# Performance work log

Hardware: AMD Instinct MI355X
Metric: run time of the kernel (lower is better)

## Reference

```python
import jax, jax.numpy as jnp
import numpy as np

B, S, H = 2, 1024, 2048
NH, NOPE, ROPE, VD = 16, 128, 64, 128
QKD = NOPE + ROPE  # 192
QLR, KVLR = 1536, 512
EPS = 1e-5


def _ln(x, w):
    # torch F.layer_norm with weight, no bias
    m = jnp.mean(x, axis=-1, keepdims=True)
    v = jnp.mean(jnp.square(x - m), axis=-1, keepdims=True)
    return (x - m) * jax.lax.rsqrt(v + EPS) * w


def _rope(x, cos, sin):
    x1, x2 = jnp.split(x, 2, axis=-1)
    return x * cos + jnp.concatenate((-x2, x1), axis=-1) * sin


def setup_inputs() -> dict:
    key = jax.random.key(0)
    ks = jax.random.split(key, 10)
    sd = 0.02
    return {
        "hidden_states": jax.random.normal(ks[0], (B, S, H), jnp.float32),
        "cos": jax.random.uniform(ks[1], (B, S, ROPE), jnp.float32),
        "sin": jax.random.uniform(ks[2], (B, S, ROPE), jnp.float32),
        "w_qa": jax.random.normal(ks[3], (QLR, H), jnp.float32) * sd,
        "q_a_ln_w": jnp.ones((QLR,), jnp.float32),
        "w_qb": jax.random.normal(ks[4], (NH * QKD, QLR), jnp.float32) * sd,
        "w_kva": jax.random.normal(ks[5], (KVLR + ROPE, H), jnp.float32) * sd,
        "kv_a_ln_w": jnp.ones((KVLR,), jnp.float32),
        "W_UK_T": jax.random.normal(ks[6], (NH, NOPE, KVLR), jnp.float32) * sd,
        "W_UV": jax.random.normal(ks[7], (NH, KVLR, VD), jnp.float32) * sd,
        "w_o": jax.random.normal(ks[8], (H, NH * VD), jnp.float32) * sd,
    }


def reference(hidden_states, cos, sin, w_qa, q_a_ln_w, w_qb, w_kva, kv_a_ln_w,
              W_UK_T, W_UV, w_o):
    b, s, _ = hidden_states.shape
    # fused mlapo: low-rank Q path + LN + RoPE
    qa = _ln(hidden_states @ w_qa.T, q_a_ln_w)            # [b,s,QLR]
    q = (qa @ w_qb.T).reshape(b, s, NH, QKD)              # [b,s,h,192]
    q_nope, q_pe = q[..., :NOPE], q[..., NOPE:]
    q_pe = _rope(q_pe, cos[:, :, None, :], sin[:, :, None, :])
    # KV low-rank path (MQA latent) + LN + RoPE on shared k_pe
    kva = hidden_states @ w_kva.T                          # [b,s,KVLR+ROPE]
    kv_c = _ln(kva[..., :KVLR], kv_a_ln_w)                 # [b,s,KVLR]
    k_pe = _rope(kva[..., KVLR:], cos, sin)                # [b,s,ROPE]
    # absorbed latent attention
    q_lat = jnp.einsum('bshd,hdl->bshl', q_nope, W_UK_T)   # [b,s,h,KVLR]
    scores = (jnp.einsum('bqhl,bkl->bhqk', q_lat, kv_c)
              + jnp.einsum('bqhr,bkr->bhqk', q_pe, k_pe)) * (1.0 / np.sqrt(QKD))
    mask = jnp.tril(jnp.ones((s, s), bool))
    scores = jnp.where(mask, scores, jnp.finfo(scores.dtype).min)
    p = jax.nn.softmax(scores, axis=-1)                    # [b,h,q,k]
    ctx = jnp.einsum('bhqk,bkl->bqhl', p, kv_c)            # [b,s,h,KVLR]
    out = jnp.einsum('bqhl,hlv->bqhv', ctx, W_UV)          # [b,s,h,VD]
    return out.reshape(b, s, NH * VD) @ w_o.T              # [b,s,H]
```

## Files before the change

### kernel.cpp

```cpp
#include <hip/hip_runtime.h>
#include <hip/hip_bf16.h>
#include <math.h>

#define BB 2
#define SS 1024
#define HH 2048
#define NHD 16
#define NOPE 128
#define ROPED 64
#define VDIM 128
#define QKD 192
#define QLR 1536
#define KVLR 512
#define EPSF 1e-5f
#define NCOMB 2176

typedef __bf16 bf16x8 __attribute__((ext_vector_type(8)));
typedef float  f32x4  __attribute__((ext_vector_type(4)));

__device__ __forceinline__ void gload_lds16(const __bf16* g, __bf16* l) {
    __builtin_amdgcn_global_load_lds(
        (const __attribute__((address_space(1))) void*)g,
        (__attribute__((address_space(3))) void*)l, 16, 0, 0);
}

__device__ __forceinline__ void swz2d(int nx, int ny, int& bx, int& by) {
    int T = nx * ny;
    int lin = blockIdx.x + nx * blockIdx.y;
    if ((T & 7) == 0) {
        int q = T >> 3;
        lin = (lin & 7) * q + (lin >> 3);
    }
    bx = lin % nx;
    by = lin / nx;
}

template<int BK>
__device__ __forceinline__ void gemm_core_dbuf(
    const __bf16* __restrict__ Ab, const __bf16* __restrict__ Bb,
    int lda, int ldb, int m0, int n0, int K, __bf16* lds, f32x4 acc[4][4])
{
    constexpr int CH    = BK / 8;
    constexpr int LPT   = CH / 2;
    constexpr int BUFE  = 256 * BK;
    constexpr int BOFF  = 128 * BK;
    constexpr int RSTEP = 2048 / BK;
    const int tid = threadIdx.x;
    const int w = tid >> 6, lane = tid & 63, quad = lane >> 4, ln = lane & 15;
    const int wm = (w >> 1) * 64, wn = (w & 1) * 64;
    const int nt = K / BK;

    const int sr  = tid / CH;
    const int spc = tid % CH;
    const int sc  = (BK == 64) ? (spc ^ (sr & 7)) : (spc ^ ((sr >> 1) & 3));
    const __bf16* gA = Ab + (size_t)(m0 + sr) * lda + sc * 8;
    const __bf16* gB = Bb + (size_t)(n0 + sr) * ldb + sc * 8;

    const int swm = (BK == 64) ? ((wm + ln) & 7) : (((wm + ln) >> 1) & 3);
    const int swn = (BK == 64) ? ((wn + ln) & 7) : (((wn + ln) >> 1) & 3);

    auto stage = [&](int buf, int kk) {
        __bf16* la = lds + buf * BUFE + w * 512;
        __bf16* lb = la + BOFF;
        const __bf16* ga = gA + kk;
        const __bf16* gb = gB + kk;
#pragma unroll
        for (int i = 0; i < LPT; ++i) {
            gload_lds16(ga + (size_t)(i * RSTEP) * lda, la + i * 2048);
            gload_lds16(gb + (size_t)(i * RSTEP) * ldb, lb + i * 2048);
        }
    };
    auto wait_stage = [&]() {
        if constexpr (BK == 64) asm volatile("s_waitcnt vmcnt(8)" ::: "memory");
        else                    asm volatile("s_waitcnt vmcnt(4)" ::: "memory");
    };

    stage(0, 0);
    stage(1, BK);
    wait_stage();
    __builtin_amdgcn_s_barrier();
    __builtin_amdgcn_sched_barrier(0);

    for (int t = 0; t < nt; ++t) {
        const int cur = t & 1;
        const __bf16* bufA = lds + cur * BUFE;
        const __bf16* bufB = bufA + BOFF;
        bf16x8 af[BK / 32][4], bv[BK / 32][4];
#pragma unroll
        for (int ks = 0; ks < BK / 32; ++ks)
#pragma unroll
            for (int i = 0; i < 4; ++i) {
                af[ks][i] = *(const bf16x8*)
                    &bufA[(wm + ln) * BK + i * 16 * BK + (((ks * 4 + quad) ^ swm) << 3)];
                bv[ks][i] = *(const bf16x8*)
                    &bufB[(wn + ln) * BK + i * 16 * BK + (((ks * 4 + quad) ^ swn) << 3)];
            }
        __builtin_amdgcn_s_setprio(1);
#pragma unroll
        for (int ks = 0; ks < BK / 32; ++ks)
#pragma unroll
            for (int mi = 0; mi < 4; ++mi)
#pragma unroll
                for (int ni = 0; ni < 4; ++ni)
                    acc[mi][ni] = __builtin_amdgcn_mfma_f32_16x16x32_bf16(
                        af[ks][mi], bv[ks][ni], acc[mi][ni], 0, 0, 0);
        __builtin_amdgcn_s_setprio(0);
        if (t + 1 < nt) {
            __builtin_amdgcn_sched_barrier(0);
            asm volatile("" ::: "memory");
            __builtin_amdgcn_s_barrier();
            asm volatile("" ::: "memory");
            if (t + 2 < nt) {
                stage(cur, (t + 2) * BK);
                wait_stage();
            } else {
                asm volatile("s_waitcnt vmcnt(0)" ::: "memory");
            }
            __builtin_amdgcn_s_barrier();
            __builtin_amdgcn_sched_barrier(0);
        }
    }
}

template<int BK>
__device__ __forceinline__ void gemm_core_tri(
    const __bf16* __restrict__ Ab, const __bf16* __restrict__ Bb,
    int lda, int ldb, int m0, int n0, int K, __bf16* lds, f32x4 acc[4][4])
{
    constexpr int CH    = BK / 8;
    constexpr int LPT   = CH / 2;
    constexpr int BUFE  = 256 * BK;
    constexpr int BOFF  = 128 * BK;
    constexpr int RSTEP = 2048 / BK;
    const int tid = threadIdx.x;
    const int w = tid >> 6, lane = tid & 63, quad = lane >> 4, ln = lane & 15;
    const int wm = (w >> 1) * 64, wn = (w & 1) * 64;
    const int nt = K / BK;

    const int sr  = tid / CH;
    const int spc = tid % CH;
    const int sc  = (BK == 64) ? (spc ^ (sr & 7)) : (spc ^ ((sr >> 1) & 3));
    const __bf16* gA = Ab + (size_t)(m0 + sr) * lda + sc * 8;
    const __bf16* gB = Bb + (size_t)(n0 + sr) * ldb + sc * 8;

    const int swm = (BK == 64) ? ((wm + ln) & 7) : (((wm + ln) >> 1) & 3);
    const int swn = (BK == 64) ? ((wn + ln) & 7) : (((wn + ln) >> 1) & 3);

    auto stage = [&](__bf16* base, int kk) {
        __bf16* la = base + w * 512;
        __bf16* lb = la + BOFF;
        const __bf16* ga = gA + kk;
        const __bf16* gb = gB + kk;
#pragma unroll
        for (int i = 0; i < LPT; ++i) {
            gload_lds16(ga + (size_t)(i * RSTEP) * lda, la + i * 2048);
            gload_lds16(gb + (size_t)(i * RSTEP) * ldb, lb + i * 2048);
        }
    };

    __bf16* p0 = lds;
    __bf16* p1 = lds + BUFE;
    __bf16* p2 = lds + 2 * BUFE;

    stage(p0, 0);
    stage(p1, BK);
    if constexpr (BK == 64) asm volatile("s_waitcnt vmcnt(8)" ::: "memory");
    else                    asm volatile("s_waitcnt vmcnt(4)" ::: "memory");
    __builtin_amdgcn_s_barrier();
    __builtin_amdgcn_sched_barrier(0);

    for (int t = 0; t < nt; ++t) {
        if (t + 2 < nt) stage(p2, (t + 2) * BK);
        bf16x8 af[BK / 32][4], bv[BK / 32][4];
#pragma unroll
        for (int ks = 0; ks < BK / 32; ++ks)
#pragma unroll
            for (int i = 0; i < 4; ++i) {
                af[ks][i] = *(const bf16x8*)
                    &p0[(wm + ln) * BK + i * 16 * BK + (((ks * 4 + quad) ^ swm) << 3)];
                bv[ks][i] = *(const bf16x8*)
                    &p0[BOFF + (wn + ln) * BK + i * 16 * BK + (((ks * 4 + quad) ^ swn) << 3)];
            }
        __builtin_amdgcn_s_setprio(1);
#pragma unroll
        for (int ks = 0; ks < BK / 32; ++ks)
#pragma unroll
            for (int mi = 0; mi < 4; ++mi)
#pragma unroll
                for (int ni = 0; ni < 4; ++ni)
                    acc[mi][ni] = __builtin_amdgcn_mfma_f32_16x16x32_bf16(
                        af[ks][mi], bv[ks][ni], acc[mi][ni], 0, 0, 0);
        __builtin_amdgcn_s_setprio(0);
        if (t + 1 < nt) {
            __builtin_amdgcn_sched_barrier(0);
            if (t + 2 < nt) {
                if constexpr (BK == 64) asm volatile("s_waitcnt vmcnt(8)" ::: "memory");
                else                    asm volatile("s_waitcnt vmcnt(4)" ::: "memory");
            } else {
                asm volatile("s_waitcnt vmcnt(0)" ::: "memory");
            }
            __builtin_amdgcn_s_barrier();
            __builtin_amdgcn_sched_barrier(0);
        }
        __bf16* tmp = p0; p0 = p1; p1 = p2; p2 = tmp;
    }
}

template<bool OUT_BF16, int BK, int MINW, bool TRI>
__global__ __launch_bounds__(256, MINW) void gemm_mfma(
    const __bf16* __restrict__ A, const __bf16* __restrict__ B, void* __restrict__ Cv,
    int M, int N, int K, int lda, int ldb, int ldc,
    long long sA, long long sB, long long sC)
{
    __shared__ __bf16 lds[TRI ? 768 * BK : 512 * BK];
    const __bf16* Ab = A + (long long)blockIdx.z * sA;
    const __bf16* Bb = B + (long long)blockIdx.z * sB;
    const int tid = threadIdx.x;
    const int w = tid >> 6, lane = tid & 63, quad = lane >> 4, ln = lane & 15;
    int bx, by; swz2d(gridDim.x, gridDim.y, bx, by);
    const int m0 = by * 128, n0 = bx * 128;
    const int wm = (w >> 1) * 64, wn = (w & 1) * 64;

    f32x4 acc[4][4];
#pragma unroll
    for (int i = 0; i < 4; ++i)
#pragma unroll
        for (int j = 0; j < 4; ++j) acc[i][j] = (f32x4){0.f, 0.f, 0.f, 0.f};

    if (TRI) gemm_core_tri<BK>(Ab, Bb, lda, ldb, m0, n0, K, lds, acc);
    else     gemm_core_dbuf<BK>(Ab, Bb, lda, ldb, m0, n0, K, lds, acc);

    if (OUT_BF16) {
        __bf16* Cb = (__bf16*)Cv + (long long)blockIdx.z * sC;
#pragma unroll
        for (int mi = 0; mi < 4; ++mi)
#pragma unroll
            for (int r = 0; r < 4; ++r) {
                size_t row = (size_t)(m0 + wm + mi * 16 + quad * 4 + r);
#pragma unroll
                for (int ni = 0; ni < 4; ++ni)
                    Cb[row * ldc + (n0 + wn + ni * 16 + ln)] = (__bf16)acc[mi][ni][r];
            }
    } else {
        float* Cb = (float*)Cv + (long long)blockIdx.z * sC;
#pragma unroll
        for (int mi = 0; mi < 4; ++mi)
#pragma unroll
            for (int r = 0; r < 4; ++r) {
                size_t row = (size_t)(m0 + wm + mi * 16 + quad * 4 + r);
#pragma unroll
                for (int ni = 0; ni < 4; ++ni)
                    Cb[row * ldc + (n0 + wn + ni * 16 + ln)] = acc[mi][ni][r];
            }
    }
}

__global__ __launch_bounds__(256, 3) void gemm_qlat(
    const __bf16* __restrict__ qb, const __bf16* __restrict__ Wkb,
    __bf16* __restrict__ Qc)
{
    __shared__ __bf16 lds[768 * 32];
    const int h = blockIdx.z;
    const __bf16* Ab = qb + (size_t)h * QKD;
    const __bf16* Bb = Wkb + (size_t)h * KVLR * NOPE;
    const int tid = threadIdx.x;
    const int w = tid >> 6, lane = tid & 63, quad = lane >> 4, ln = lane & 15;
    int bx, by; swz2d(gridDim.x, gridDim.y, bx, by);
    const int m0 = by * 128, n0 = bx * 128;
    const int wm = (w >> 1) * 64, wn = (w & 1) * 64;

    f32x4 acc[4][4];
#pragma unroll
    for (int i = 0; i < 4; ++i)
#pragma unroll
        for (int j = 0; j < 4; ++j) acc[i][j] = (f32x4){0.f, 0.f, 0.f, 0.f};

    gemm_core_tri<32>(Ab, Bb, NHD * QKD, NOPE, m0, n0, NOPE, lds, acc);

#pragma unroll
    for (int mi = 0; mi < 4; ++mi)
#pragma unroll
        for (int r = 0; r < 4; ++r) {
            int row = m0 + wm + mi * 16 + quad * 4 + r;
            int bb = row >> 10, s = row & 1023;
            __bf16* dst = Qc + ((size_t)(bb * NHD + h) * SS + s) * 576;
#pragma unroll
            for (int ni = 0; ni < 4; ++ni)
                dst[n0 + wn + ni * 16 + ln] = (__bf16)acc[mi][ni][r];
        }
}

__global__ __launch_bounds__(256, 3) void gemm_vh(
    const __bf16* __restrict__ Wvb, const __bf16* __restrict__ Kc,
    __bf16* __restrict__ Vh)
{
    int lin = blockIdx.x + 8 * blockIdx.z;
    lin = (lin & 7) * 32 + (lin >> 3);
    const int z = lin >> 3;
    const int ntile = lin & 7;
    const int b = z >> 4, h = z & 15;

    __shared__ __bf16 lds[768 * 32];
    const __bf16* Ab = Wvb + (size_t)h * VDIM * KVLR;
    const __bf16* Bb = Kc + (size_t)b * SS * 576;
    const int tid = threadIdx.x;
    const int w = tid >> 6, lane = tid & 63, quad = lane >> 4, ln = lane & 15;
    const int m0 = 0, n0 = ntile * 128;
    const int wm = (w >> 1) * 64, wn = (w & 1) * 64;

    f32x4 acc[4][4];
#pragma unroll
    for (int i = 0; i < 4; ++i)
#pragma unroll
        for (int j = 0; j < 4; ++j) acc[i][j] = (f32x4){0.f, 0.f, 0.f, 0.f};

    gemm_core_tri<32>(Ab, Bb, KVLR, 576, m0, n0, KVLR, lds, acc);

    __bf16* Cb = Vh + (size_t)z * VDIM * SS;
#pragma unroll
    for (int mi = 0; mi < 4; ++mi)
#pragma unroll
        for (int r = 0; r < 4; ++r) {
            int row = m0 + wm + mi * 16 + quad * 4 + r;
#pragma unroll
            for (int ni = 0; ni < 4; ++ni)
                Cb[(size_t)row * SS + (n0 + wn + ni * 16 + ln)] = (__bf16)acc[mi][ni][r];
        }
}

__global__ __launch_bounds__(256, 3) void gemm_scores(
    const __bf16* __restrict__ Qc, const __bf16* __restrict__ Kc,
    __bf16* __restrict__ Sc)
{
    int lin = blockIdx.x + 36 * blockIdx.y;
    lin = (lin & 7) * 144 + (lin >> 3);
    const int z = lin / 36;
    const int i = lin - z * 36;
    int mt = (int)((sqrtf(8.f * i + 1.f) - 1.f) * 0.5f);
    if (mt * (mt + 1) / 2 > i) --mt;
    if ((mt + 1) * (mt + 2) / 2 <= i) ++mt;
    const int nt = i - mt * (mt + 1) / 2;

    const int b = z >> 4;
    __shared__ __bf16 lds[768 * 32];
    const __bf16* Ab = Qc + (size_t)z * SS * 576;
    const __bf16* Bb = Kc + (size_t)b * SS * 576;
    __bf16* Cb = Sc + (size_t)z * SS * SS;
    const int tid = threadIdx.x;
    const int w = tid >> 6, lane = tid & 63, quad = lane >> 4, ln = lane & 15;
    const int m0 = mt * 128, n0 = nt * 128;
    const int wm = (w >> 1) * 64, wn = (w & 1) * 64;

    f32x4 acc[4][4];
#pragma unroll
    for (int i2 = 0; i2 < 4; ++i2)
#pragma unroll
        for (int j = 0; j < 4; ++j) acc[i2][j] = (f32x4){0.f, 0.f, 0.f, 0.f};

    gemm_core_tri<32>(Ab, Bb, 576, 576, m0, n0, 576, lds, acc);

    const float SCL2 = 0.07216878364870323f * 1.4426950408889634f;
#pragma unroll
    for (int mi = 0; mi < 4; ++mi)
#pragma unroll
        for (int r = 0; r < 4; ++r) {
            int row = m0 + wm + mi * 16 + quad * 4 + r;
#pragma unroll
            for (int ni = 0; ni < 4; ++ni) {
                int col = n0 + wn + ni * 16 + ln;
                float v = acc[mi][ni][r] * SCL2;
                if (col > row) v = -1e30f;
                Cb[(size_t)row * SS + col] = (__bf16)v;
            }
        }
}

__global__ __launch_bounds__(256) void softmax_kernel(__bf16* __restrict__ Sc)
{
    const int z = blockIdx.y;
    const int w = threadIdx.x >> 6, lane = threadIdx.x & 63;
    const int r = blockIdx.x * 4 + w;
    __bf16* row = Sc + (size_t)z * SS * SS + (size_t)r * SS;
    const int ncols = ((r >> 7) + 1) << 7;
    const int i0 = lane * 8, i1 = i0 + 512;
    const bool a0 = i0 < ncols, a1 = i1 < ncols;
    float v[16];
    float lmax = -1e30f;
    if (a0) {
        bf16x8 c = *(const bf16x8*)(row + i0);
#pragma unroll
        for (int j = 0; j < 8; ++j) { v[j] = (float)c[j]; lmax = fmaxf(lmax, v[j]); }
    }
    if (a1) {
        bf16x8 c = *(const bf16x8*)(row + i1);
#pragma unroll
        for (int j = 0; j < 8; ++j) { v[8 + j] = (float)c[j]; lmax = fmaxf(lmax, v[8 + j]); }
    }
#pragma unroll
    for (int off = 1; off < 64; off <<= 1) lmax = fmaxf(lmax, __shfl_xor(lmax, off));
    float lsum = 0.f;
    if (a0) {
#pragma unroll
        for (int j = 0; j < 8; ++j) { v[j] = __builtin_amdgcn_exp2f(v[j] - lmax); lsum += v[j]; }
    }
    if (a1) {
#pragma unroll
        for (int j = 0; j < 8; ++j) { v[8 + j] = __builtin_amdgcn_exp2f(v[8 + j] - lmax); lsum += v[8 + j]; }
    }
#pragma unroll
    for (int off = 1; off < 64; off <<= 1) lsum += __shfl_xor(lsum, off);
    const float inv = 1.f / lsum;
    if (a0) {
        bf16x8 c;
#pragma unroll
        for (int j = 0; j < 8; ++j) c[j] = (__bf16)(v[j] * inv);
        *(bf16x8*)(row + i0) = c;
    }
    if (a1) {
        bf16x8 c;
#pragma unroll
        for (int j = 0; j < 8; ++j) c[j] = (__bf16)(v[8 + j] * inv);
        *(bf16x8*)(row + i1) = c;
    }
}

__global__ __launch_bounds__(256, 3) void gemm_pv(
    const __bf16* __restrict__ Sc, const __bf16* __restrict__ Vh,
    __bf16* __restrict__ ohb)
{
    int lin = blockIdx.x + 8 * blockIdx.y;
    lin = (lin & 7) * 32 + (lin >> 3);
    const int z = lin >> 3;
    const int mt = lin & 7;

    const int b = z >> 4, h = z & 15;
    const int Keff = (mt + 1) * 128;
    __shared__ __bf16 lds[768 * 32];
    const __bf16* Ab = Sc + (size_t)z * SS * SS;
    const __bf16* Bb = Vh + (size_t)z * VDIM * SS;
    const int tid = threadIdx.x;
    const int w = tid >> 6, lane = tid & 63, quad = lane >> 4, ln = lane & 15;
    const int m0 = mt * 128, n0 = 0;
    const int wm = (w >> 1) * 64, wn = (w & 1) * 64;

    f32x4 acc[4][4];
#pragma unroll
    for (int i = 0; i < 4; ++i)
#pragma unroll
        for (int j = 0; j < 4; ++j) acc[i][j] = (f32x4){0.f, 0.f, 0.f, 0.f};

    gemm_core_tri<32>(Ab, Bb, SS, SS, m0, n0, Keff, lds, acc);

#pragma unroll
    for (int mi = 0; mi < 4; ++mi)
#pragma unroll
        for (int r = 0; r < 4; ++r) {
            int row = m0 + wm + mi * 16 + quad * 4 + r;
            __bf16* op = ohb + (size_t)(b * SS + row) * (NHD * VDIM) + h * VDIM;
#pragma unroll
            for (int ni = 0; ni < 4; ++ni)
                op[n0 + wn + ni * 16 + ln] = (__bf16)acc[mi][ni][r];
        }
}

__global__ __launch_bounds__(256) void castf2b(const float* __restrict__ in,
                                               __bf16* __restrict__ out, int n)
{
    int i = (blockIdx.x * 256 + threadIdx.x) * 4;
    if (i < n) {
        float4 v = *(const float4*)(in + i);
        out[i] = (__bf16)v.x; out[i + 1] = (__bf16)v.y;
        out[i + 2] = (__bf16)v.z; out[i + 3] = (__bf16)v.w;
    }
}

__global__ __launch_bounds__(256) void cast_comb(const float* __restrict__ wqa,
                                                 const float* __restrict__ wkva,
                                                 __bf16* __restrict__ out)
{
    int idx = (blockIdx.x * 256 + threadIdx.x) * 4;
    int row = idx >> 11, col = idx & 2047;
    const float* src;
    if (row < 1536)      src = wqa + (size_t)row * 2048 + col;
    else if (row < 2112) src = wkva + (size_t)(row - 1536) * 2048 + col;
    else {
        out[idx] = (__bf16)0.f; out[idx + 1] = (__bf16)0.f;
        out[idx + 2] = (__bf16)0.f; out[idx + 3] = (__bf16)0.f;
        return;
    }
    float4 v = *(const float4*)src;
    out[idx] = (__bf16)v.x; out[idx + 1] = (__bf16)v.y;
    out[idx + 2] = (__bf16)v.z; out[idx + 3] = (__bf16)v.w;
}

__global__ __launch_bounds__(256) void transpose_cast(const float* __restrict__ in,
                                                      __bf16* __restrict__ out,
                                                      int R, int C)
{
    __shared__ float t[32][33];
    in  += (size_t)blockIdx.z * R * C;
    out += (size_t)blockIdx.z * R * C;
    int c0 = blockIdx.x * 32, r0 = blockIdx.y * 32;
    int tx = threadIdx.x & 31, ty = threadIdx.x >> 5;
#pragma unroll
    for (int i = 0; i < 4; ++i) {
        int r = ty + i * 8;
        t[r][tx] = in[(size_t)(r0 + r) * C + c0 + tx];
    }
    __syncthreads();
#pragma unroll
    for (int i = 0; i < 4; ++i) {
        int rr = ty + i * 8;
        out[(size_t)(c0 + rr) * R + r0 + tx] = (__bf16)t[tx][rr];
    }
}

__global__ __launch_bounds__(256) void ln_kernel(const float* __restrict__ x,
                                                 const float* __restrict__ w,
                                                 __bf16* __restrict__ y, int N, int ldx)
{
    long long row = blockIdx.x;
    const float* xr = x + row * ldx;
    __bf16* yr = y + row * N;
    int tid = threadIdx.x;
    float s = 0.f, ss = 0.f;
    for (int i = tid; i < N; i += 256) { float v = xr[i]; s += v; ss += v * v; }
#pragma unroll
    for (int off = 32; off > 0; off >>= 1) { s += __shfl_down(s, off); ss += __shfl_down(ss, off); }
    __shared__ float rs[4], rss[4];
    __shared__ float smean, sinv;
    int wave = tid >> 6, lane = tid & 63;
    if (lane == 0) { rs[wave] = s; rss[wave] = ss; }
    __syncthreads();
    if (tid == 0) {
        float S = rs[0] + rs[1] + rs[2] + rs[3];
        float Q = rss[0] + rss[1] + rss[2] + rss[3];
        float mean = S / N;
        float var = Q / N - mean * mean;
        smean = mean; sinv = rsqrtf(var + EPSF);
    }
    __syncthreads();
    float mean = smean, inv = sinv;
    for (int i = tid; i < N; i += 256) yr[i] = (__bf16)((xr[i] - mean) * inv * w[i]);
}

__global__ __launch_bounds__(256) void prep_kernel(
    const float* __restrict__ kva, int ld, const float* __restrict__ kvw,
    const float* __restrict__ cosb, const float* __restrict__ sinb,
    __bf16* __restrict__ Kc, const __bf16* __restrict__ q,
    __bf16* __restrict__ Qc)
{
    long long row = blockIdx.x;
    const float* kr = kva + row * ld;
    const float* cr = cosb + row * ROPED;
    const float* sr = sinb + row * ROPED;
    int tid = threadIdx.x;
    float v0 = kr[tid], v1 = kr[tid + 256];
    float s = v0 + v1, ss = v0 * v0 + v1 * v1;
#pragma unroll
    for (int off = 32; off > 0; off >>= 1) { s += __shfl_down(s, off); ss += __shfl_down(ss, off); }
    __shared__ float rs[4], rss[4];
    __shared__ float smean, sinv;
    int wave = tid >> 6, lane = tid & 63;
    if (lane == 0) { rs[wave] = s; rss[wave] = ss; }
    __syncthreads();
    if (tid == 0) {
        float S = rs[0] + rs[1] + rs[2] + rs[3];
        float Q = rss[0] + rss[1] + rss[2] + rss[3];
        float mean = S / KVLR;
        float var = Q / KVLR - mean * mean;
        smean = mean; sinv = rsqrtf(var + EPSF);
    }
    __syncthreads();
    float mean = smean, inv = sinv;
    __bf16* kc = Kc + row * 576;
    kc[tid]       = (__bf16)((v0 - mean) * inv * kvw[tid]);
    kc[tid + 256] = (__bf16)((v1 - mean) * inv * kvw[tid + 256]);
    if (tid < 32) {
        float x1 = kr[KVLR + tid], x2 = kr[KVLR + 32 + tid];
        kc[512 + tid]      = (__bf16)(x1 * cr[tid] - x2 * sr[tid]);
        kc[512 + 32 + tid] = (__bf16)(x2 * cr[32 + tid] + x1 * sr[32 + tid]);
    }
    const int bb = (int)(row >> 10), sp = (int)(row & 1023);
    const __bf16* qr = q + row * (NHD * QKD);
#pragma unroll
    for (int j = 0; j < 2; ++j) {
        int idx = tid + j * 256;
        int h = idx >> 5, p = idx & 31;
        const __bf16* base = qr + h * QKD + NOPE;
        float x1 = (float)base[p], x2 = (float)base[32 + p];
        __bf16* qcb = Qc + ((size_t)(bb * NHD + h) * SS + sp) * 576 + 512;
        qcb[p]      = (__bf16)(x1 * cr[p] - x2 * sr[p]);
        qcb[32 + p] = (__bf16)(x2 * cr[32 + p] + x1 * sr[32 + p]);
    }
}

extern "C" void kernel_launch(void* const* d_in, const int* in_sizes, int n_in,
                              void* d_out, int out_size, void* d_ws, size_t ws_size,
                              hipStream_t stream)
{
    const float* hidden    = (const float*)d_in[0];
    const float* cosb      = (const float*)d_in[1];
    const float* sinb      = (const float*)d_in[2];
    const float* w_qa      = (const float*)d_in[3];
    const float* q_a_ln_w  = (const float*)d_in[4];
    const float* w_qb      = (const float*)d_in[5];
    const float* w_kva     = (const float*)d_in[6];
    const float* kv_a_ln_w = (const float*)d_in[7];
    const float* W_UK_T    = (const float*)d_in[8];
    const float* W_UV      = (const float*)d_in[9];
    const float* w_o       = (const float*)d_in[10];
    float* out = (float*)d_out;

    const int M = BB * SS;
    float*  qakva = (float*)d_ws;
    __bf16* Xb    = (__bf16*)(qakva + (size_t)M * NCOMB);
    __bf16* qab   = Xb    + (size_t)M * HH;
    __bf16* qb    = qab   + (size_t)M * QLR;
    __bf16* qlatb = qb    + (size_t)M * NHD * QKD;
    __bf16* Sc    = (__bf16*)d_ws;
    __bf16* Kc    = qlatb + (size_t)M * NHD * KVLR;
    __bf16* Qc    = Kc    + (size_t)M * 576;
    __bf16* Vt    = Qc    + (size_t)M * NHD * 576;
    __bf16* ctxb  = Vt    + (size_t)BB * 512 * SS;
    __bf16* Vh    = ctxb;
    __bf16* ohb   = ctxb  + (size_t)M * NHD * KVLR;
    __bf16* w_cmb = ohb   + (size_t)M * HH;
    __bf16* w_qbb = w_cmb + (size_t)NCOMB * HH;
    __bf16* Wkb   = w_qbb + (size_t)NHD * QKD * QLR;
    __bf16* Wvb   = Wkb   + (size_t)NHD * KVLR * NOPE;
    __bf16* w_ob  = Wvb   + (size_t)NHD * VDIM * KVLR;

    dim3 blk(256);

    castf2b<<<dim3((M * HH) / 1024), blk, 0, stream>>>(hidden, Xb, M * HH);
    cast_comb<<<dim3((NCOMB * HH) / 1024), blk, 0, stream>>>(w_qa, w_kva, w_cmb);
    castf2b<<<dim3((NHD * QKD * QLR) / 1024), blk, 0, stream>>>(w_qb, w_qbb, NHD * QKD * QLR);
    castf2b<<<dim3((HH * HH) / 1024), blk, 0, stream>>>(w_o, w_ob, HH * HH);
    transpose_cast<<<dim3(KVLR / 32, NOPE / 32, NHD), blk, 0, stream>>>(W_UK_T, Wkb, NOPE, KVLR);
    transpose_cast<<<dim3(VDIM / 32, KVLR / 32, NHD), blk, 0, stream>>>(W_UV, Wvb, KVLR, VDIM);

    gemm_mfma<false, 64, 2, false><<<dim3(NCOMB / 128, M / 128, 1), blk, 0, stream>>>(
        Xb, w_cmb, qakva, M, NCOMB, HH, HH, HH, NCOMB, 0, 0, 0);
    ln_kernel<<<dim3(M), blk, 0, stream>>>(qakva, q_a_ln_w, qab, QLR, NCOMB);
    gemm_mfma<true, 64, 2, false><<<dim3(NHD * QKD / 128, M / 128, 1), blk, 0, stream>>>(
        qab, w_qbb, qb, M, NHD * QKD, QLR, QLR, QLR, NHD * QKD, 0, 0, 0);
    prep_kernel<<<dim3(M), blk, 0, stream>>>(qakva + QLR, NCOMB, kv_a_ln_w,
                                             cosb, sinb, Kc, qb, Qc);
    gemm_vh<<<dim3(8, 1, 32), blk, 0, stream>>>(Wvb, Kc, Vh);
    gemm_qlat<<<dim3(KVLR / 128, M / 128, NHD), blk, 0, stream>>>(qb, Wkb, Qc);
    gemm_scores<<<dim3(36, 32), blk, 0, stream>>>(Qc, Kc, Sc);
    softmax_kernel<<<dim3(SS / 4, 32), blk, 0, stream>>>(Sc);
    gemm_pv<<<dim3(8, 32), blk, 0, stream>>>(Sc, Vh, ohb);
    gemm_mfma<false, 64, 2, false><<<dim3(HH / 128, M / 128, 1), blk, 0, stream>>>(
        ohb, w_ob, out, M, HH, NHD * VDIM, NHD * VDIM, NHD * VDIM, HH, 0, 0, 0);
}
```

Before: 312.2 us.

## Un-absorb key projection: compute per-head K from latent, shrink score GEMM to 192

Instead of absorbing W_UK into the queries (producing a 576-wide per-head Q latent), the new path projects the shared latent KV through W_UK per head into a 192-wide per-head key (nope part plus the rotated k_pe). The score GEMM then contracts over 192 instead of 576, and the query-latent GEMM is replaced by a per-head key GEMM of the same shape class. RoPE for q is applied in place in qb, and W_UK_T is now cast without a transpose. This is meant to cut score-GEMM FLOPs and Q-side memory traffic, at the cost of materializing per-head keys and writing k_pe replicated per head.

```diff
diff --git a/kernel.cpp b/kernel.cpp
--- a/kernel.cpp
+++ b/kernel.cpp
@@ -255,18 +255,22 @@
     }
 }
 
-__global__ __launch_bounds__(256, 3) void gemm_qlat(
-    const __bf16* __restrict__ qb, const __bf16* __restrict__ Wkb,
-    __bf16* __restrict__ Qc)
-{
+__global__ __launch_bounds__(256, 3) void gemm_kh(
+    const __bf16* __restrict__ Kc, const __bf16* __restrict__ Wuk,
+    __bf16* __restrict__ Khb)
+{
+    int lin = blockIdx.x + 8 * blockIdx.z;
+    lin = (lin & 7) * 32 + (lin >> 3);
+    const int z = lin >> 3;
+    const int mt = lin & 7;
+    const int b = z >> 4, h = z & 15;
+
     __shared__ __bf16 lds[768 * 32];
-    const int h = blockIdx.z;
-    const __bf16* Ab = qb + (size_t)h * QKD;
-    const __bf16* Bb = Wkb + (size_t)h * KVLR * NOPE;
+    const __bf16* Ab = Kc + (size_t)b * SS * 576;
+    const __bf16* Bb = Wuk + (size_t)h * NOPE * KVLR;
     const int tid = threadIdx.x;
     const int w = tid >> 6, lane = tid & 63, quad = lane >> 4, ln = lane & 15;
-    int bx, by; swz2d(gridDim.x, gridDim.y, bx, by);
-    const int m0 = by * 128, n0 = bx * 128;
+    const int m0 = mt * 128, n0 = 0;
     const int wm = (w >> 1) * 64, wn = (w & 1) * 64;
 
     f32x4 acc[4][4];
@@ -275,18 +279,17 @@
 #pragma unroll
         for (int j = 0; j < 4; ++j) acc[i][j] = (f32x4){0.f, 0.f, 0.f, 0.f};
 
-    gemm_core_tri<32>(Ab, Bb, NHD * QKD, NOPE, m0, n0, NOPE, lds, acc);
-
+    gemm_core_tri<32>(Ab, Bb, 576, KVLR, m0, n0, KVLR, lds, acc);
+
+    __bf16* Cb = Khb + (size_t)z * SS * QKD;
 #pragma unroll
     for (int mi = 0; mi < 4; ++mi)
 #pragma unroll
         for (int r = 0; r < 4; ++r) {
             int row = m0 + wm + mi * 16 + quad * 4 + r;
-            int bb = row >> 10, s = row & 1023;
-            __bf16* dst = Qc + ((size_t)(bb * NHD + h) * SS + s) * 576;
 #pragma unroll
             for (int ni = 0; ni < 4; ++ni)
-                dst[n0 + wn + ni * 16 + ln] = (__bf16)acc[mi][ni][r];
+                Cb[(size_t)row * QKD + (n0 + wn + ni * 16 + ln)] = (__bf16)acc[mi][ni][r];
         }
 }
 
@@ -329,7 +332,7 @@
 }
 
 __global__ __launch_bounds__(256, 3) void gemm_scores(
-    const __bf16* __restrict__ Qc, const __bf16* __restrict__ Kc,
+    const __bf16* __restrict__ qb, const __bf16* __restrict__ Khb,
     __bf16* __restrict__ Sc)
 {
     int lin = blockIdx.x + 36 * blockIdx.y;
@@ -341,10 +344,10 @@
     if ((mt + 1) * (mt + 2) / 2 <= i) ++mt;
     const int nt = i - mt * (mt + 1) / 2;
 
-    const int b = z >> 4;
+    const int b = z >> 4, h = z & 15;
     __shared__ __bf16 lds[768 * 32];
-    const __bf16* Ab = Qc + (size_t)z * SS * 576;
-    const __bf16* Bb = Kc + (size_t)b * SS * 576;
+    const __bf16* Ab = qb + (size_t)b * SS * (NHD * QKD) + (size_t)h * QKD;
+    const __bf16* Bb = Khb + (size_t)z * SS * QKD;
     __bf16* Cb = Sc + (size_t)z * SS * SS;
     const int tid = threadIdx.x;
     const int w = tid >> 6, lane = tid & 63, quad = lane >> 4, ln = lane & 15;
@@ -357,7 +360,7 @@
 #pragma unroll
         for (int j = 0; j < 4; ++j) acc[i2][j] = (f32x4){0.f, 0.f, 0.f, 0.f};
 
-    gemm_core_tri<32>(Ab, Bb, 576, 576, m0, n0, 576, lds, acc);
+    gemm_core_tri<32>(Ab, Bb, NHD * QKD, QKD, m0, n0, QKD, lds, acc);
 
     const float SCL2 = 0.07216878364870323f * 1.4426950408889634f;
 #pragma unroll
@@ -547,8 +550,8 @@
 __global__ __launch_bounds__(256) void prep_kernel(
     const float* __restrict__ kva, int ld, const float* __restrict__ kvw,
     const float* __restrict__ cosb, const float* __restrict__ sinb,
-    __bf16* __restrict__ Kc, const __bf16* __restrict__ q,
-    __bf16* __restrict__ Qc)
+    __bf16* __restrict__ Kc, __bf16* __restrict__ q,
+    __bf16* __restrict__ Khb)
 {
     long long row = blockIdx.x;
     const float* kr = kva + row * ld;
@@ -561,6 +564,7 @@
     for (int off = 32; off > 0; off >>= 1) { s += __shfl_down(s, off); ss += __shfl_down(ss, off); }
     __shared__ float rs[4], rss[4];
     __shared__ float smean, sinv;
+    __shared__ float kpe_s[64];
     int wave = tid >> 6, lane = tid & 63;
     if (lane == 0) { rs[wave] = s; rss[wave] = ss; }
     __syncthreads();
@@ -578,20 +582,30 @@
     kc[tid + 256] = (__bf16)((v1 - mean) * inv * kvw[tid + 256]);
     if (tid < 32) {
         float x1 = kr[KVLR + tid], x2 = kr[KVLR + 32 + tid];
-        kc[512 + tid]      = (__bf16)(x1 * cr[tid] - x2 * sr[tid]);
-        kc[512 + 32 + tid] = (__bf16)(x2 * cr[32 + tid] + x1 * sr[32 + tid]);
+        float r1 = x1 * cr[tid] - x2 * sr[tid];
+        float r2 = x2 * cr[32 + tid] + x1 * sr[32 + tid];
+        kc[512 + tid]      = (__bf16)r1;
+        kc[512 + 32 + tid] = (__bf16)r2;
+        kpe_s[tid]      = r1;
+        kpe_s[32 + tid] = r2;
     }
     const int bb = (int)(row >> 10), sp = (int)(row & 1023);
-    const __bf16* qr = q + row * (NHD * QKD);
+    __bf16* qr = q + row * (NHD * QKD);
 #pragma unroll
     for (int j = 0; j < 2; ++j) {
         int idx = tid + j * 256;
         int h = idx >> 5, p = idx & 31;
-        const __bf16* base = qr + h * QKD + NOPE;
+        __bf16* base = qr + h * QKD + NOPE;
         float x1 = (float)base[p], x2 = (float)base[32 + p];
-        __bf16* qcb = Qc + ((size_t)(bb * NHD + h) * SS + sp) * 576 + 512;
-        qcb[p]      = (__bf16)(x1 * cr[p] - x2 * sr[p]);
-        qcb[32 + p] = (__bf16)(x2 * cr[32 + p] + x1 * sr[32 + p]);
+        base[p]      = (__bf16)(x1 * cr[p] - x2 * sr[p]);
+        base[32 + p] = (__bf16)(x2 * cr[32 + p] + x1 * sr[32 + p]);
+    }
+    __syncthreads();
+#pragma unroll
+    for (int j = 0; j < 4; ++j) {
+        int idx = tid + j * 256;
+        int h = idx >> 6, c = idx & 63;
+        Khb[((size_t)(bb * NHD + h) * SS + sp) * QKD + NOPE + c] = (__bf16)kpe_s[c];
     }
 }
 
@@ -616,19 +630,16 @@
     float*  qakva = (float*)d_ws;
     __bf16* Xb    = (__bf16*)(qakva + (size_t)M * NCOMB);
     __bf16* qab   = Xb    + (size_t)M * HH;
-    __bf16* qb    = qab   + (size_t)M * QLR;
-    __bf16* qlatb = qb    + (size_t)M * NHD * QKD;
     __bf16* Sc    = (__bf16*)d_ws;
-    __bf16* Kc    = qlatb + (size_t)M * NHD * KVLR;
-    __bf16* Qc    = Kc    + (size_t)M * 576;
-    __bf16* Vt    = Qc    + (size_t)M * NHD * 576;
-    __bf16* ctxb  = Vt    + (size_t)BB * 512 * SS;
-    __bf16* Vh    = ctxb;
-    __bf16* ohb   = ctxb  + (size_t)M * NHD * KVLR;
+    __bf16* qb    = Sc    + (size_t)32 * SS * SS;
+    __bf16* Kc    = qb    + (size_t)M * NHD * QKD;
+    __bf16* Khb   = Kc    + (size_t)M * 576;
+    __bf16* Vh    = Khb   + (size_t)32 * SS * QKD;
+    __bf16* ohb   = Vh    + (size_t)32 * VDIM * SS;
     __bf16* w_cmb = ohb   + (size_t)M * HH;
     __bf16* w_qbb = w_cmb + (size_t)NCOMB * HH;
     __bf16* Wkb   = w_qbb + (size_t)NHD * QKD * QLR;
-    __bf16* Wvb   = Wkb   + (size_t)NHD * KVLR * NOPE;
+    __bf16* Wvb   = Wkb   + (size_t)NHD * NOPE * KVLR;
     __bf16* w_ob  = Wvb   + (size_t)NHD * VDIM * KVLR;
 
     dim3 blk(256);
@@ -637,7 +648,7 @@
     cast_comb<<<dim3((NCOMB * HH) / 1024), blk, 0, stream>>>(w_qa, w_kva, w_cmb);
     castf2b<<<dim3((NHD * QKD * QLR) / 1024), blk, 0, stream>>>(w_qb, w_qbb, NHD * QKD * QLR);
     castf2b<<<dim3((HH * HH) / 1024), blk, 0, stream>>>(w_o, w_ob, HH * HH);
-    transpose_cast<<<dim3(KVLR / 32, NOPE / 32, NHD), blk, 0, stream>>>(W_UK_T, Wkb, NOPE, KVLR);
+    castf2b<<<dim3((NHD * NOPE * KVLR) / 1024), blk, 0, stream>>>(W_UK_T, Wkb, NHD * NOPE * KVLR);
     transpose_cast<<<dim3(VDIM / 32, KVLR / 32, NHD), blk, 0, stream>>>(W_UV, Wvb, KVLR, VDIM);
 
     gemm_mfma<false, 64, 2, false><<<dim3(NCOMB / 128, M / 128, 1), blk, 0, stream>>>(
@@ -646,10 +657,10 @@
     gemm_mfma<true, 64, 2, false><<<dim3(NHD * QKD / 128, M / 128, 1), blk, 0, stream>>>(
         qab, w_qbb, qb, M, NHD * QKD, QLR, QLR, QLR, NHD * QKD, 0, 0, 0);
     prep_kernel<<<dim3(M), blk, 0, stream>>>(qakva + QLR, NCOMB, kv_a_ln_w,
-                                             cosb, sinb, Kc, qb, Qc);
+                                             cosb, sinb, Kc, qb, Khb);
     gemm_vh<<<dim3(8, 1, 32), blk, 0, stream>>>(Wvb, Kc, Vh);
-    gemm_qlat<<<dim3(KVLR / 128, M / 128, NHD), blk, 0, stream>>>(qb, Wkb, Qc);
-    gemm_scores<<<dim3(36, 32), blk, 0, stream>>>(Qc, Kc, Sc);
+    gemm_kh<<<dim3(8, 1, 32), blk, 0, stream>>>(Kc, Wkb, Khb);
+    gemm_scores<<<dim3(36, 32), blk, 0, stream>>>(qb, Khb, Sc);
     softmax_kernel<<<dim3(SS / 4, 32), blk, 0, stream>>>(Sc);
     gemm_pv<<<dim3(8, 32), blk, 0, stream>>>(Sc, Vh, ohb);
     gemm_mfma<false, 64, 2, false><<<dim3(HH / 128, M / 128, 1), blk, 0, stream>>>(
```

Measured after the change: 298.8 us. 1.04x faster.
